# Kernel tuning notes

Measured on AMD Instinct MI355X. Metric: run time of the kernel, lower is better.

Reference implementation:

```python
import jax, jax.numpy as jnp
import numpy as np

EPS = 1e-12  # F.normalize default eps

def _l1_normalize(x, axis):
    return x / jnp.maximum(jnp.sum(jnp.abs(x), axis=axis, keepdims=True), EPS)


def setup_inputs() -> dict:
    key = jax.random.key(0)
    k1, k2, k3, k4 = jax.random.split(key, 4)
    B_src, S_src, d = 4096, 32, 512
    B_tgt, T = 32, 256
    m = jax.random.normal(k1, (B_src, S_src, d), dtype=jnp.float32)
    om = jax.random.normal(k2, (B_tgt, T, d), dtype=jnp.float32)
    src_mask = jax.random.randint(k3, (B_src, 1, S_src), 0, 2, dtype=jnp.int32)
    tgt_mask = jax.random.randint(k4, (B_tgt, T, T), 0, 2, dtype=jnp.int32)
    return {"m": m, "om": om, "src_mask": src_mask, "tgt_mask": tgt_mask}


def reference(m, om, src_mask, tgt_mask):
    # masked mean readouts (L1-normalized masks as attention weights)
    src_w = _l1_normalize(src_mask.astype(jnp.float32), axis=-1)      # [B_src,1,S_src]
    src_readout = jnp.einsum('bos,bsd->bod', src_w, m)[:, 0, :]       # [B_src,d]
    tgt_w = _l1_normalize(tgt_mask.astype(jnp.float32), axis=-1)      # [B_tgt,T,T]
    tgt_readout = jnp.einsum('btu,bud->btd', tgt_w, om)               # [B_tgt,T,d]

    # pairwise L2 distance over d WITHOUT materializing [B_tgt,T,B_src,d]:
    # ||t - s||^2 = ||t||^2 + ||s||^2 - 2 t.s
    t_sq = jnp.sum(tgt_readout * tgt_readout, axis=-1)                # [B_tgt,T]
    s_sq = jnp.sum(src_readout * src_readout, axis=-1)                # [B_src]
    cross = jnp.einsum('btd,nd->btn', tgt_readout, src_readout)       # [B_tgt,T,B_src]
    d2 = t_sq[..., None] + s_sq[None, None, :] - 2.0 * cross
    dist = jnp.sqrt(jnp.maximum(d2, EPS))
    sim = jnp.exp(-dist)
    sim = _l1_normalize(sim, axis=-1)                                 # [B_tgt,T,B_src]
    return sim
```

## Files before the change

kernel.cpp:

```cpp
#include <hip/hip_runtime.h>
#include <math.h>

#define EPSF 1e-12f

typedef short bf16x8 __attribute__((ext_vector_type(8)));
typedef float f32x4 __attribute__((ext_vector_type(4)));

__device__ __forceinline__ void gload_lds16(const void* g, void* l) {
  __builtin_amdgcn_global_load_lds(
      (const __attribute__((address_space(1))) unsigned int*)g,
      (__attribute__((address_space(3))) unsigned int*)l, 16, 0, 0);
}

__device__ __forceinline__ unsigned short bf16_rne(float f) {
  unsigned int u = __float_as_uint(f);
  u += 0x7fffu + ((u >> 16) & 1u);
  return (unsigned short)(u >> 16);
}

__device__ __forceinline__ float bf16_to_f32(unsigned short h) {
  return __uint_as_float((unsigned int)h << 16);
}

__device__ __forceinline__ float block_reduce_sum_256(float v) {
#pragma unroll
  for (int o = 32; o > 0; o >>= 1) v += __shfl_down(v, o, 64);
  __shared__ float ws4[4];
  const int lane = threadIdx.x & 63;
  const int w = threadIdx.x >> 6;
  if (lane == 0) ws4[w] = v;
  __syncthreads();
  if (threadIdx.x == 0) ws4[0] = ws4[0] + ws4[1] + ws4[2] + ws4[3];
  __syncthreads();
  return ws4[0];
}

__global__ __launch_bounds__(256) void k_src_readout(const float* __restrict__ m,
                                                     const int* __restrict__ src_mask,
                                                     unsigned short* __restrict__ srcRb,
                                                     float* __restrict__ ssq) {
  const int tid = threadIdx.x;
  const int sub = tid >> 7, t = tid & 127;
  const int b = blockIdx.x * 2 + sub;
  __shared__ int msk[2][32];
  __shared__ float sinv[2];
  __shared__ float red[4];
  if (t < 32) msk[sub][t] = src_mask[b * 32 + t];
  __syncthreads();
  if (t == 0) {
    float c = 0.f;
    for (int s = 0; s < 32; ++s) c += (float)msk[sub][s];
    sinv[sub] = 1.0f / fmaxf(c, EPSF);
  }
  __syncthreads();
  const float inv = sinv[sub];
  const float4* mb = (const float4*)(m + (size_t)b * (32 * 512)) + t;
  float ax = 0.f, ay = 0.f, az = 0.f, aw = 0.f;
  for (int s = 0; s < 32; ++s) {
    if (msk[sub][s] != 0) {
      float4 v = mb[s * 128];
      ax += v.x; ay += v.y; az += v.z; aw += v.w;
    }
  }
  ushort4 o;
  o.x = bf16_rne(ax * inv);
  o.y = bf16_rne(ay * inv);
  o.z = bf16_rne(az * inv);
  o.w = bf16_rne(aw * inv);
  *(ushort4*)(srcRb + (size_t)b * 512 + t * 4) = o;
  float fx = bf16_to_f32(o.x), fy = bf16_to_f32(o.y);
  float fz = bf16_to_f32(o.z), fw = bf16_to_f32(o.w);
  float s = fx * fx + fy * fy + fz * fz + fw * fw;
#pragma unroll
  for (int oo = 32; oo > 0; oo >>= 1) s += __shfl_down(s, oo, 64);
  if ((tid & 63) == 0) red[tid >> 6] = s;
  __syncthreads();
  if (t == 0) ssq[b] = red[sub * 2] + red[sub * 2 + 1];
}

#define WST 72
__global__ __launch_bounds__(512) void k_tgt_readout_mfma(
    const float* __restrict__ om, const int* __restrict__ tgt_mask,
    unsigned short* __restrict__ Afrag) {
  const int b = blockIdx.x, dq = blockIdx.y, th = blockIdx.z;
  const int d0 = dq * 128, t0 = th * 128;
  __shared__ unsigned short Wb[128 * WST];
  __shared__ unsigned short omT[128 * WST];
  __shared__ float cntp[128 * 4];
  __shared__ float cnt_inv[128];
  const int tid = threadIdx.x;
  const int lane = tid & 63, w = tid >> 6;
  const int* mbase = tgt_mask + (size_t)b * 65536 + (size_t)t0 * 256;

  {
    const int t = tid >> 2, q = tid & 3;
    const int* mp = mbase + t * 256 + q * 64;
    int c = 0;
#pragma unroll
    for (int k = 0; k < 16; ++k) {
      int4 v = *(const int4*)(mp + 4 * k);
      c += v.x + v.y + v.z + v.w;
    }
    cntp[t * 4 + q] = (float)c;
  }
  __syncthreads();
  if (tid < 128) {
    float c = cntp[tid * 4] + cntp[tid * 4 + 1] + cntp[tid * 4 + 2] + cntp[tid * 4 + 3];
    cnt_inv[tid] = 1.0f / fmaxf(c, EPSF);
  }

  f32x4 acc[8];
#pragma unroll
  for (int di = 0; di < 8; ++di) acc[di] = (f32x4){0.f, 0.f, 0.f, 0.f};

  for (int uc = 0; uc < 4; ++uc) {
    const int ub = uc * 64;
    __syncthreads();
    {
      const int t = tid >> 2, ul0 = (tid & 3) * 16;
      const int* mp = mbase + t * 256 + ub + ul0;
      unsigned short* wp = Wb + t * WST + ul0;
#pragma unroll
      for (int k = 0; k < 4; ++k) {
        int4 v = *(const int4*)(mp + 4 * k);
        ushort4 h;
        h.x = v.x ? 0x3F80 : 0;
        h.y = v.y ? 0x3F80 : 0;
        h.z = v.z ? 0x3F80 : 0;
        h.w = v.w ? 0x3F80 : 0;
        *(ushort4*)(wp + 4 * k) = h;
      }
    }
    {
#pragma unroll
      for (int k = 0; k < 4; ++k) {
        const int idx = tid + 512 * k;
        const int u = idx >> 5, dl = (idx & 31) * 4;
        float4 v = *(const float4*)(om + (size_t)b * 131072 + (size_t)(ub + u) * 512 + d0 + dl);
        omT[(dl + 0) * WST + u] = bf16_rne(v.x);
        omT[(dl + 1) * WST + u] = bf16_rne(v.y);
        omT[(dl + 2) * WST + u] = bf16_rne(v.z);
        omT[(dl + 3) * WST + u] = bf16_rne(v.w);
      }
    }
    __syncthreads();
#pragma unroll
    for (int kt2 = 0; kt2 < 2; ++kt2) {
      const int ko = kt2 * 32 + (lane >> 4) * 8;
      bf16x8 wf = *(const bf16x8*)(Wb + (w * 16 + (lane & 15)) * WST + ko);
      bf16x8 of[8];
#pragma unroll
      for (int di = 0; di < 8; ++di)
        of[di] = *(const bf16x8*)(omT + (di * 16 + (lane & 15)) * WST + ko);
#pragma unroll
      for (int di = 0; di < 8; ++di)
        acc[di] = __builtin_amdgcn_mfma_f32_16x16x32_bf16(of[di], wf, acc[di], 0, 0, 0);
    }
  }

  const int tl = w * 16 + (lane & 15);
  const int rT = b * 256 + t0 + tl;
  const float inv = cnt_inv[tl];
#pragma unroll
  for (int di = 0; di < 8; ++di) {
    const int d = d0 + di * 16 + (lane >> 4) * 4;
    ushort4 o;
    o.x = bf16_rne(acc[di][0] * inv);
    o.y = bf16_rne(acc[di][1] * inv);
    o.z = bf16_rne(acc[di][2] * inv);
    o.w = bf16_rne(acc[di][3] * inv);
    const size_t off =
        (((size_t)(rT >> 4) * 16 + (d >> 5)) * 64 + ((d >> 3) & 3) * 16 + (rT & 15)) * 8 + (d & 7);
    *(ushort4*)(Afrag + off) = o;
  }
}

__global__ __launch_bounds__(256) void k_rowsq_frag(const unsigned short* __restrict__ Afrag,
                                                    float* __restrict__ sq) {
  const int r = blockIdx.x;
  const int tid = threadIdx.x;
  const int g = r >> 4, rl = r & 15;
  const int d = 2 * tid;
  const size_t off = ((size_t)((g * 16 + (d >> 5)) * 64 + ((d >> 3) & 3) * 16 + rl)) * 8 + (d & 7);
  ushort2 v = *(const ushort2*)(Afrag + off);
  float fx = bf16_to_f32(v.x), fy = bf16_to_f32(v.y);
  float s = fx * fx + fy * fy;
  s = block_reduce_sum_256(s);
  if (tid == 0) sq[r] = s;
}

__global__ __launch_bounds__(512, 4) void k_cross_mfma(
    const unsigned short* __restrict__ Afrag, const unsigned short* __restrict__ B,
    const float* __restrict__ tsq, const float* __restrict__ ssq,
    float* __restrict__ out) {
  __shared__ unsigned short Bs[64 * 512];
  const int tid = threadIdx.x;
  const int lane = tid & 63, w = tid >> 6;
  const int row0 = blockIdx.y * 512, col0 = blockIdx.x * 64;
  const int lr = lane & 15, lkh = lane >> 4;

#pragma unroll
  for (int t = 0; t < 8; ++t) {
    const int c = w * 8 + t;
    const int cb = c >> 4, kt = c & 15;
    gload_lds16(B + (size_t)(col0 + cb * 16 + lr) * 512 + kt * 32 + lkh * 8,
                Bs + (size_t)c * 512);
  }

  f32x4 acc[4][4];
#pragma unroll
  for (int i = 0; i < 4; ++i)
#pragma unroll
    for (int j = 0; j < 4; ++j) acc[i][j] = (f32x4){0.f, 0.f, 0.f, 0.f};

  __syncthreads();

  const unsigned short* ap = Afrag + ((size_t)(row0 >> 4) + w * 4) * (16 * 64 * 8);
#pragma unroll
  for (int kt = 0; kt < 16; ++kt) {
    bf16x8 af[4], bfr[4];
#pragma unroll
    for (int i = 0; i < 4; ++i)
      af[i] = *(const bf16x8*)(ap + (((size_t)i * 16 + kt) * 64 + lane) * 8);
#pragma unroll
    for (int j = 0; j < 4; ++j)
      bfr[j] = *(const bf16x8*)(Bs + ((j * 16 + kt) * 64 + lane) * 8);
#pragma unroll
    for (int i = 0; i < 4; ++i)
#pragma unroll
      for (int j = 0; j < 4; ++j)
        acc[i][j] = __builtin_amdgcn_mfma_f32_16x16x32_bf16(af[i], bfr[j], acc[i][j], 0, 0, 0);
  }

  const int cbase = col0 + (lane & 15);
  const int rbase = row0 + w * 64 + (lane >> 4) * 4;
  float ss[4];
#pragma unroll
  for (int j = 0; j < 4; ++j) ss[j] = ssq[cbase + j * 16];
#pragma unroll
  for (int i = 0; i < 4; ++i) {
#pragma unroll
    for (int r = 0; r < 4; ++r) {
      const int row = rbase + i * 16 + r;
      const float t2 = tsq[row];
      float* op = out + (size_t)row * 4096 + cbase;
#pragma unroll
      for (int j = 0; j < 4; ++j) {
        float d2 = t2 + ss[j] - 2.0f * acc[i][j][r];
        op[j * 16] = expf(-sqrtf(fmaxf(d2, EPSF)));
      }
    }
  }
}

__global__ __launch_bounds__(256) void k_norm(float* __restrict__ out) {
  const size_t base = (size_t)blockIdx.x * 4096;
  const int tid = threadIdx.x;
  float4 v[4];
  float s = 0.f;
#pragma unroll
  for (int i = 0; i < 4; ++i) {
    v[i] = *(const float4*)(out + base + (size_t)(tid * 4 + i * 1024));
    s += v[i].x + v[i].y + v[i].z + v[i].w;
  }
  s = block_reduce_sum_256(s);
  const float inv = 1.0f / fmaxf(s, EPSF);
#pragma unroll
  for (int i = 0; i < 4; ++i) {
    float4 r;
    r.x = v[i].x * inv;
    r.y = v[i].y * inv;
    r.z = v[i].z * inv;
    r.w = v[i].w * inv;
    *(float4*)(out + base + (size_t)(tid * 4 + i * 1024)) = r;
  }
}

extern "C" void kernel_launch(void* const* d_in, const int* in_sizes, int n_in,
                              void* d_out, int out_size, void* d_ws, size_t ws_size,
                              hipStream_t stream) {
  const float* m = (const float*)d_in[0];
  const float* om = (const float*)d_in[1];
  const int* src_mask = (const int*)d_in[2];
  const int* tgt_mask = (const int*)d_in[3];
  float* out = (float*)d_out;

  float* ws = (float*)d_ws;
  float* ssq = ws;
  float* tsq = ssq + 4096;
  unsigned short* srcRb = (unsigned short*)(tsq + 8192);
  unsigned short* Afrag = srcRb + 4096 * 512;

  k_src_readout<<<2048, 256, 0, stream>>>(m, src_mask, srcRb, ssq);
  k_tgt_readout_mfma<<<dim3(32, 4, 2), 512, 0, stream>>>(om, tgt_mask, Afrag);
  k_rowsq_frag<<<8192, 256, 0, stream>>>(Afrag, tsq);
  k_cross_mfma<<<dim3(64, 16), 512, 0, stream>>>(Afrag, srcRb, tsq, ssq, out);
  k_norm<<<8192, 256, 0, stream>>>(out);
}
```

Before: 171.1 us.

## Retile cross-distance GEMM to 128x128 blocks with per-k LDS staging and nontemporal stores

The cross GEMM kernel moves from 512-row x 64-col blocks of 8 waves, which preload a 64-column B panel for all of K into 64KB of LDS, to 128x128 blocks of 4 waves in a 2x2 layout. Each k-step now stages a small B slice in LDS, bracketed by two barriers. This raises the grid from 1024 to 2048 blocks, shrinks the LDS footprint and lets each B slice be shared by two wave columns, at the cost of per-iteration synchronisation and no prefetch overlap. The output stores in both the cross and normalisation kernels become nontemporal to reduce cache pollution from the large output.

```diff
diff --git a/kernel.cpp b/kernel.cpp
--- a/kernel.cpp
+++ b/kernel.cpp
@@ -189,42 +189,43 @@
   if (tid == 0) sq[r] = s;
 }
 
-__global__ __launch_bounds__(512, 4) void k_cross_mfma(
+__global__ __launch_bounds__(256, 3) void k_cross_mfma(
     const unsigned short* __restrict__ Afrag, const unsigned short* __restrict__ B,
     const float* __restrict__ tsq, const float* __restrict__ ssq,
     float* __restrict__ out) {
-  __shared__ unsigned short Bs[64 * 512];
+  __shared__ unsigned short Bs[8 * 512];
   const int tid = threadIdx.x;
   const int lane = tid & 63, w = tid >> 6;
-  const int row0 = blockIdx.y * 512, col0 = blockIdx.x * 64;
+  const int wm = w >> 1, wn = w & 1;
+  const int col0 = blockIdx.x * 128, row0 = blockIdx.y * 128;
   const int lr = lane & 15, lkh = lane >> 4;
 
-#pragma unroll
-  for (int t = 0; t < 8; ++t) {
-    const int c = w * 8 + t;
-    const int cb = c >> 4, kt = c & 15;
-    gload_lds16(B + (size_t)(col0 + cb * 16 + lr) * 512 + kt * 32 + lkh * 8,
-                Bs + (size_t)c * 512);
-  }
-
   f32x4 acc[4][4];
 #pragma unroll
   for (int i = 0; i < 4; ++i)
 #pragma unroll
     for (int j = 0; j < 4; ++j) acc[i][j] = (f32x4){0.f, 0.f, 0.f, 0.f};
 
-  __syncthreads();
-
-  const unsigned short* ap = Afrag + ((size_t)(row0 >> 4) + w * 4) * (16 * 64 * 8);
-#pragma unroll
+  const size_t arb0 = (size_t)(row0 >> 4) + wm * 4;
+
   for (int kt = 0; kt < 16; ++kt) {
-    bf16x8 af[4], bfr[4];
+    const int kb = kt * 32;
+    bf16x8 af[4];
 #pragma unroll
     for (int i = 0; i < 4; ++i)
-      af[i] = *(const bf16x8*)(ap + (((size_t)i * 16 + kt) * 64 + lane) * 8);
+      af[i] = *(const bf16x8*)(Afrag + ((arb0 + i) * 16 + kt) * 512 + lane * 8);
+    __syncthreads();
+#pragma unroll
+    for (int t = 0; t < 2; ++t) {
+      const int c = w * 2 + t;
+      gload_lds16(B + (size_t)(col0 + c * 16 + lr) * 512 + kb + lkh * 8,
+                  Bs + (size_t)c * 512);
+    }
+    __syncthreads();
+    bf16x8 bfr[4];
 #pragma unroll
     for (int j = 0; j < 4; ++j)
-      bfr[j] = *(const bf16x8*)(Bs + ((j * 16 + kt) * 64 + lane) * 8);
+      bfr[j] = *(const bf16x8*)(Bs + ((wn * 4 + j) * 64 + lane) * 8);
 #pragma unroll
     for (int i = 0; i < 4; ++i)
 #pragma unroll
@@ -232,8 +233,8 @@
         acc[i][j] = __builtin_amdgcn_mfma_f32_16x16x32_bf16(af[i], bfr[j], acc[i][j], 0, 0, 0);
   }
 
-  const int cbase = col0 + (lane & 15);
-  const int rbase = row0 + w * 64 + (lane >> 4) * 4;
+  const int cbase = col0 + wn * 64 + (lane & 15);
+  const int rbase = row0 + wm * 64 + (lane >> 4) * 4;
   float ss[4];
 #pragma unroll
   for (int j = 0; j < 4; ++j) ss[j] = ssq[cbase + j * 16];
@@ -247,7 +248,7 @@
 #pragma unroll
       for (int j = 0; j < 4; ++j) {
         float d2 = t2 + ss[j] - 2.0f * acc[i][j][r];
-        op[j * 16] = expf(-sqrtf(fmaxf(d2, EPSF)));
+        __builtin_nontemporal_store(expf(-sqrtf(fmaxf(d2, EPSF))), op + j * 16);
       }
     }
   }
@@ -267,12 +268,12 @@
   const float inv = 1.0f / fmaxf(s, EPSF);
 #pragma unroll
   for (int i = 0; i < 4; ++i) {
-    float4 r;
-    r.x = v[i].x * inv;
-    r.y = v[i].y * inv;
-    r.z = v[i].z * inv;
-    r.w = v[i].w * inv;
-    *(float4*)(out + base + (size_t)(tid * 4 + i * 1024)) = r;
+    f32x4 r;
+    r[0] = v[i].x * inv;
+    r[1] = v[i].y * inv;
+    r[2] = v[i].z * inv;
+    r[3] = v[i].w * inv;
+    __builtin_nontemporal_store(r, (f32x4*)(out + base + (size_t)(tid * 4 + i * 1024)));
   }
 }
 
@@ -294,6 +295,6 @@
   k_src_readout<<<2048, 256, 0, stream>>>(m, src_mask, srcRb, ssq);
   k_tgt_readout_mfma<<<dim3(32, 4, 2), 512, 0, stream>>>(om, tgt_mask, Afrag);
   k_rowsq_frag<<<8192, 256, 0, stream>>>(Afrag, tsq);
-  k_cross_mfma<<<dim3(64, 16), 512, 0, stream>>>(Afrag, srcRb, tsq, ssq, out);
+  k_cross_mfma<<<dim3(32, 64), 256, 0, stream>>>(Afrag, srcRb, tsq, ssq, out);
   k_norm<<<8192, 256, 0, stream>>>(out);
 }
```

Measured after the change: 179.4 us. 1.05x slower.
